# Kernel tuning notes

Measured on AMD Instinct MI355X. Metric: run time of the kernel, lower is better.

Reference implementation:

```python
import jax, jax.numpy as jnp
import numpy as np

N_NODES = 100000
N_EDGES = 1600000
IN_CH, HID_CH, OUT_CH = 128, 128, 64


def _sage_conv(x, src, dst, Wl, bl, Wr, num_nodes):
    # PyG SAGEConv (aggr='mean', root_weight=True):
    #   out_i = W_l @ mean_{j in N(i)} x_j + b_l + W_r @ x_i
    msgs = x[src]                                            # [E, d] gather
    agg = jax.ops.segment_sum(msgs, dst, num_segments=num_nodes)   # [N, d]
    cnt = jax.ops.segment_sum(jnp.ones((src.shape[0],), x.dtype), dst,
                              num_segments=num_nodes)              # [N]
    mean = agg / jnp.maximum(cnt, 1.0)[:, None]
    return mean @ Wl.T + bl + x @ Wr.T


def setup_inputs() -> dict:
    key = jax.random.key(0)
    ks = jax.random.split(key, 8)
    x = jax.random.normal(ks[0], (N_NODES, IN_CH), dtype=jnp.float32)
    edge_index = jax.random.randint(ks[1], (2, N_EDGES), 0, N_NODES, dtype=jnp.int32)
    s1 = 1.0 / np.sqrt(IN_CH)
    s2 = 1.0 / np.sqrt(HID_CH)
    Wl1 = jax.random.uniform(ks[2], (HID_CH, IN_CH), jnp.float32, -s1, s1)
    bl1 = jax.random.uniform(ks[3], (HID_CH,), jnp.float32, -s1, s1)
    Wr1 = jax.random.uniform(ks[4], (HID_CH, IN_CH), jnp.float32, -s1, s1)
    Wl2 = jax.random.uniform(ks[5], (OUT_CH, HID_CH), jnp.float32, -s2, s2)
    bl2 = jax.random.uniform(ks[6], (OUT_CH,), jnp.float32, -s2, s2)
    Wr2 = jax.random.uniform(ks[7], (OUT_CH, HID_CH), jnp.float32, -s2, s2)
    return {"x": x, "edge_index": edge_index, "Wl1": Wl1, "bl1": bl1,
            "Wr1": Wr1, "Wl2": Wl2, "bl2": bl2, "Wr2": Wr2}


def reference(x, edge_index, Wl1, bl1, Wr1, Wl2, bl2, Wr2):
    src, dst = edge_index[0], edge_index[1]
    n = x.shape[0]
    h = _sage_conv(x, src, dst, Wl1, bl1, Wr1, n)
    h = jax.nn.relu(h)  # dropout is identity in eval mode
    out = _sage_conv(h, src, dst, Wl2, bl2, Wr2, n)
    return out
```

## Files before the change

### kernel.cpp

```cpp
#include <hip/hip_runtime.h>
#include <hip/hip_bf16.h>
#include <stdint.h>

#define IN_CH 128
#define NPB   448
#define NBUCK 224
#define CAP   8192
#define PART_EPB 2048
#define SRC_BITS 17
#define SRC_MASK ((1 << SRC_BITS) - 1)

typedef short v8s __attribute__((ext_vector_type(8)));
typedef float v4f __attribute__((ext_vector_type(4)));

__device__ __forceinline__ ushort f2b(float f) {
    return ((__hip_bfloat16_raw)__float2bfloat16(f)).x;
}
__device__ __forceinline__ float b2f(ushort u) {
    __hip_bfloat16_raw r; r.x = u;
    return __bfloat162float((__hip_bfloat16)r);
}

__global__ __launch_bounds__(256) void k_part(
    const int* __restrict__ src, const int* __restrict__ dst,
    int* __restrict__ cursor, int* __restrict__ ebuf, int E) {
    __shared__ int sedge[PART_EPB];
    __shared__ int h[NBUCK], lofs[NBUCK], gbase[NBUCK], lcur[NBUCK];
    __shared__ int ssc[256];

    int tid = threadIdx.x;
    int eb0 = blockIdx.x * PART_EPB;
    int cnt = min(PART_EPB, E - eb0);

    if (tid < NBUCK) { h[tid] = 0; lcur[tid] = 0; }
    __syncthreads();
    for (int i = tid; i < cnt; i += 256)
        atomicAdd(&h[dst[eb0 + i] / NPB], 1);
    __syncthreads();
    int v = (tid < NBUCK) ? h[tid] : 0;
    ssc[tid] = v;
    __syncthreads();
    for (int off = 1; off < 256; off <<= 1) {
        int val = (tid >= off) ? ssc[tid - off] : 0;
        __syncthreads();
        ssc[tid] += val;
        __syncthreads();
    }
    int excl = ssc[tid] - v;
    if (tid < NBUCK) {
        lofs[tid] = excl;
        gbase[tid] = tid * CAP + atomicAdd(&cursor[tid], v);
    }
    __syncthreads();
    for (int i = tid; i < cnt; i += 256) {
        int s0 = src[eb0 + i];
        int d0 = dst[eb0 + i];
        int b = d0 / NPB;
        int dl = d0 - b * NPB;
        int p = atomicAdd(&lcur[b], 1);
        sedge[lofs[b] + p] = (dl << SRC_BITS) | s0;
    }
    __syncthreads();
    for (int i = tid; i < cnt; i += 256) {
        int lo = 0, hi = NBUCK - 1;
        while (lo < hi) {
            int mid = (lo + hi + 1) >> 1;
            if (lofs[mid] <= i) lo = mid; else hi = mid - 1;
        }
        int pos = gbase[lo] + (i - lofs[lo]);
        if (pos < (lo + 1) * CAP) ebuf[pos] = sedge[i];
    }
}

__global__ __launch_bounds__(256) void k_bbuild(
    const int* __restrict__ ebuf, const int* __restrict__ cursor,
    int* __restrict__ row_ptr, int* __restrict__ deg,
    int* __restrict__ col, int N) {
    __shared__ int sdeg[NPB];
    __shared__ int scur[NPB];
    __shared__ int ssum[256];
    int b = blockIdx.x, tid = threadIdx.x;
    int base = b * NPB;
    int nodes = min(NPB, N - base);
    int e0 = b * CAP;
    int e1 = e0 + min(cursor[b], CAP);

    for (int i = tid; i < NPB; i += 256) sdeg[i] = 0;
    __syncthreads();
    for (int e = e0 + tid; e < e1; e += 256)
        atomicAdd(&sdeg[((unsigned)ebuf[e]) >> SRC_BITS], 1);
    __syncthreads();
    int d0 = 0, d1 = 0;
    if (tid < 224) { d0 = sdeg[2 * tid]; d1 = sdeg[2 * tid + 1]; }
    int ts = d0 + d1;
    ssum[tid] = ts;
    __syncthreads();
    for (int off = 1; off < 256; off <<= 1) {
        int val = (tid >= off) ? ssum[tid - off] : 0;
        __syncthreads();
        ssum[tid] += val;
        __syncthreads();
    }
    int excl = ssum[tid] - ts;
    if (tid < 224) {
        scur[2 * tid] = excl;
        scur[2 * tid + 1] = excl + d0;
        if (2 * tid < nodes) {
            row_ptr[base + 2 * tid] = e0 + excl;
            deg[base + 2 * tid] = d0;
        }
        if (2 * tid + 1 < nodes) {
            row_ptr[base + 2 * tid + 1] = e0 + excl + d0;
            deg[base + 2 * tid + 1] = d1;
        }
    }
    __syncthreads();
    for (int e = e0 + tid; e < e1; e += 256) {
        int w = ebuf[e];
        int dl = ((unsigned)w) >> SRC_BITS;
        int p = atomicAdd(&scur[dl], 1);
        col[e0 + p] = w & SRC_MASK;
    }
}

template <int OC, int MODE>
__global__ __launch_bounds__(256) void k_wgemm(
    const float* __restrict__ Af, const ushort* __restrict__ Ab,
    const float* __restrict__ WlF, const float* __restrict__ WrF,
    ushort* __restrict__ qb, ushort* __restrict__ pbb, float* __restrict__ pbf,
    int N) {
    const int NT = OC / 16;
    const int LDW = 128 + 8;
    __shared__ ushort Wlds[OC * LDW];

    int tid = threadIdx.x;
    for (int it = 0; it < OC / 16; it++) {
        int idx = it * 256 + tid;
        int r = idx >> 4, kc = (idx & 15) * 8;
        const float* Wrow = (r < OC / 2) ? (WlF + (size_t)r * 128)
                                         : (WrF + (size_t)(r - OC / 2) * 128);
        float4 w0 = *(const float4*)(Wrow + kc);
        float4 w1 = *(const float4*)(Wrow + kc + 4);
        v8s wv;
        wv[0] = (short)f2b(w0.x); wv[1] = (short)f2b(w0.y);
        wv[2] = (short)f2b(w0.z); wv[3] = (short)f2b(w0.w);
        wv[4] = (short)f2b(w1.x); wv[5] = (short)f2b(w1.y);
        wv[6] = (short)f2b(w1.z); wv[7] = (short)f2b(w1.w);
        *(v8s*)((short*)Wlds + r * LDW + kc) = wv;
    }
    __syncthreads();

    int wave = tid >> 6;
    int lane = tid & 63;
    int m16 = lane & 15;
    int quad = lane >> 4;
    int rowbase = blockIdx.x * 128 + wave * 32;

    v4f acc[2][NT];
#pragma unroll
    for (int mt = 0; mt < 2; mt++)
#pragma unroll
        for (int t = 0; t < NT; t++) acc[mt][t] = {0.f, 0.f, 0.f, 0.f};

    int ar0 = min(rowbase + m16, N - 1);
    int ar1 = min(rowbase + 16 + m16, N - 1);

#pragma unroll
    for (int ks = 0; ks < 4; ks++) {
        int k0 = ks * 32 + quad * 8;
        v8s a0, a1;
        if (MODE == 0) {
            float4 f00 = *(const float4*)(Af + (size_t)ar0 * 128 + k0);
            float4 f01 = *(const float4*)(Af + (size_t)ar0 * 128 + k0 + 4);
            float4 f10 = *(const float4*)(Af + (size_t)ar1 * 128 + k0);
            float4 f11 = *(const float4*)(Af + (size_t)ar1 * 128 + k0 + 4);
            a0[0] = (short)f2b(f00.x); a0[1] = (short)f2b(f00.y);
            a0[2] = (short)f2b(f00.z); a0[3] = (short)f2b(f00.w);
            a0[4] = (short)f2b(f01.x); a0[5] = (short)f2b(f01.y);
            a0[6] = (short)f2b(f01.z); a0[7] = (short)f2b(f01.w);
            a1[0] = (short)f2b(f10.x); a1[1] = (short)f2b(f10.y);
            a1[2] = (short)f2b(f10.z); a1[3] = (short)f2b(f10.w);
            a1[4] = (short)f2b(f11.x); a1[5] = (short)f2b(f11.y);
            a1[6] = (short)f2b(f11.z); a1[7] = (short)f2b(f11.w);
        } else {
            a0 = *(const v8s*)((const short*)Ab + (size_t)ar0 * 128 + k0);
            a1 = *(const v8s*)((const short*)Ab + (size_t)ar1 * 128 + k0);
        }
#pragma unroll
        for (int t = 0; t < NT; t++) {
            v8s b = *(const v8s*)((const short*)Wlds + (t * 16 + m16) * LDW + k0);
            acc[0][t] = __builtin_amdgcn_mfma_f32_16x16x32_bf16(a0, b, acc[0][t], 0, 0, 0);
            acc[1][t] = __builtin_amdgcn_mfma_f32_16x16x32_bf16(a1, b, acc[1][t], 0, 0, 0);
        }
    }

#pragma unroll
    for (int mt = 0; mt < 2; mt++) {
        int orow0 = rowbase + mt * 16 + quad * 4;
#pragma unroll
        for (int r = 0; r < 4; r++) {
            int orow = orow0 + r;
            if (orow < N) {
#pragma unroll
                for (int t = 0; t < NT; t++) {
                    int c = t * 16 + m16;
                    float v = acc[mt][t][r];
                    if (MODE == 0) {
                        if (c < 128) qb[(size_t)orow * 128 + c] = f2b(v);
                        else pbb[(size_t)orow * 128 + (c - 128)] = f2b(v);
                    } else {
                        if (c < 64) qb[(size_t)orow * 64 + c] = f2b(v);
                        else pbf[(size_t)orow * 64 + (c - 64)] = v;
                    }
                }
            }
        }
    }
}

__global__ void k_agg1(const int* __restrict__ row_ptr, const int* __restrict__ deg,
                       const int* __restrict__ col, const ushort* __restrict__ q1b,
                       const ushort* __restrict__ p1b, const float* __restrict__ bias,
                       ushort* __restrict__ hb, int N) {
    int node = blockIdx.x * (blockDim.x >> 6) + (threadIdx.x >> 6);
    int lane = threadIdx.x & 63;
    if (node >= N) return;
    int s0 = row_ptr[node];
    int dn = deg[node];
    int s1 = s0 + dn;
    int ch = 2 * lane;
    float ax = 0.f, ay = 0.f;
    int j = s0;
    for (; j + 8 <= s1; j += 8) {
        int c0 = col[j],     c1 = col[j + 1], c2 = col[j + 2], c3 = col[j + 3];
        int c4 = col[j + 4], c5 = col[j + 5], c6 = col[j + 6], c7 = col[j + 7];
        ushort2 v0 = *(const ushort2*)(q1b + (size_t)c0 * 128 + ch);
        ushort2 v1 = *(const ushort2*)(q1b + (size_t)c1 * 128 + ch);
        ushort2 v2 = *(const ushort2*)(q1b + (size_t)c2 * 128 + ch);
        ushort2 v3 = *(const ushort2*)(q1b + (size_t)c3 * 128 + ch);
        ushort2 v4 = *(const ushort2*)(q1b + (size_t)c4 * 128 + ch);
        ushort2 v5 = *(const ushort2*)(q1b + (size_t)c5 * 128 + ch);
        ushort2 v6 = *(const ushort2*)(q1b + (size_t)c6 * 128 + ch);
        ushort2 v7 = *(const ushort2*)(q1b + (size_t)c7 * 128 + ch);
        ax += b2f(v0.x) + b2f(v1.x) + b2f(v2.x) + b2f(v3.x)
            + b2f(v4.x) + b2f(v5.x) + b2f(v6.x) + b2f(v7.x);
        ay += b2f(v0.y) + b2f(v1.y) + b2f(v2.y) + b2f(v3.y)
            + b2f(v4.y) + b2f(v5.y) + b2f(v6.y) + b2f(v7.y);
    }
    for (; j < s1; j++) {
        ushort2 v = *(const ushort2*)(q1b + (size_t)col[j] * 128 + ch);
        ax += b2f(v.x); ay += b2f(v.y);
    }
    float inv = (dn > 0) ? 1.0f / (float)dn : 0.0f;
    ushort2 pb = *(const ushort2*)(p1b + (size_t)node * 128 + ch);
    float2 bi = *(const float2*)(bias + ch);
    ushort2 o;
    o.x = f2b(fmaxf(ax * inv + b2f(pb.x) + bi.x, 0.f));
    o.y = f2b(fmaxf(ay * inv + b2f(pb.y) + bi.y, 0.f));
    *(ushort2*)(hb + (size_t)node * 128 + ch) = o;
}

__global__ void k_agg2(const int* __restrict__ row_ptr, const int* __restrict__ deg,
                       const int* __restrict__ col, const ushort* __restrict__ q2,
                       const float* __restrict__ p2, const float* __restrict__ bias,
                       float* __restrict__ out, int N) {
    int node = blockIdx.x * (blockDim.x >> 6) + (threadIdx.x >> 6);
    int lane = threadIdx.x & 63;
    if (node >= N) return;
    int s0 = row_ptr[node];
    int dn = deg[node];
    int s1 = s0 + dn;
    int half = lane >> 5, cl = lane & 31;
    int ch = 2 * cl;
    float ax = 0.f, ay = 0.f;
    int j = s0;
    for (; j + 16 <= s1; j += 16) {
        int c0 = col[j + half],      c1 = col[j + 2 + half];
        int c2 = col[j + 4 + half],  c3 = col[j + 6 + half];
        int c4 = col[j + 8 + half],  c5 = col[j + 10 + half];
        int c6 = col[j + 12 + half], c7 = col[j + 14 + half];
        ushort2 v0 = *(const ushort2*)(q2 + (size_t)c0 * 64 + ch);
        ushort2 v1 = *(const ushort2*)(q2 + (size_t)c1 * 64 + ch);
        ushort2 v2 = *(const ushort2*)(q2 + (size_t)c2 * 64 + ch);
        ushort2 v3 = *(const ushort2*)(q2 + (size_t)c3 * 64 + ch);
        ushort2 v4 = *(const ushort2*)(q2 + (size_t)c4 * 64 + ch);
        ushort2 v5 = *(const ushort2*)(q2 + (size_t)c5 * 64 + ch);
        ushort2 v6 = *(const ushort2*)(q2 + (size_t)c6 * 64 + ch);
        ushort2 v7 = *(const ushort2*)(q2 + (size_t)c7 * 64 + ch);
        ax += b2f(v0.x) + b2f(v1.x) + b2f(v2.x) + b2f(v3.x)
            + b2f(v4.x) + b2f(v5.x) + b2f(v6.x) + b2f(v7.x);
        ay += b2f(v0.y) + b2f(v1.y) + b2f(v2.y) + b2f(v3.y)
            + b2f(v4.y) + b2f(v5.y) + b2f(v6.y) + b2f(v7.y);
    }
    for (; j + half < s1; j += 2) {
        ushort2 v = *(const ushort2*)(q2 + (size_t)col[j + half] * 64 + ch);
        ax += b2f(v.x); ay += b2f(v.y);
    }
    ax += __shfl_xor(ax, 32);
    ay += __shfl_xor(ay, 32);
    if (half == 0) {
        float inv = (dn > 0) ? 1.0f / (float)dn : 0.0f;
        float2 pv = *(const float2*)(p2 + (size_t)node * 64 + ch);
        float2 bi = *(const float2*)(bias + ch);
        float2 o;
        o.x = ax * inv + pv.x + bi.x;
        o.y = ay * inv + pv.y + bi.y;
        *(float2*)(out + (size_t)node * 64 + ch) = o;
    }
}

extern "C" void kernel_launch(void* const* d_in, const int* in_sizes, int n_in,
                              void* d_out, int out_size, void* d_ws, size_t ws_size,
                              hipStream_t stream) {
    const float* x   = (const float*)d_in[0];
    const int* ei    = (const int*)d_in[1];
    const float* Wl1 = (const float*)d_in[2];
    const float* bl1 = (const float*)d_in[3];
    const float* Wr1 = (const float*)d_in[4];
    const float* Wl2 = (const float*)d_in[5];
    const float* bl2 = (const float*)d_in[6];
    const float* Wr2 = (const float*)d_in[7];

    const int N = in_sizes[0] / IN_CH;
    const int E = in_sizes[1] / 2;
    const int* src = ei;
    const int* dst = ei + E;

    char* p = (char*)d_ws;
    auto carve = [&](size_t bytes) -> void* {
        void* q = (void*)p;
        p += (bytes + 255) & ~(size_t)255;
        return q;
    };
    int* cursor   = (int*)carve(NBUCK * 4);
    int* ebuf     = (int*)carve((size_t)NBUCK * CAP * 4);
    int* col      = (int*)carve((size_t)NBUCK * CAP * 4);
    int* row_ptr  = (int*)carve((size_t)N * 4);
    int* deg      = (int*)carve((size_t)N * 4);
    ushort* q1b   = (ushort*)carve((size_t)N * 128 * 2);
    ushort* p1b   = (ushort*)carve((size_t)N * 128 * 2);
    ushort* hb    = (ushort*)carve((size_t)N * 128 * 2);
    ushort* q2    = (ushort*)carve((size_t)N * 64 * 2);
    float* p2     = (float*)carve((size_t)N * 64 * 4);
    (void)ws_size; (void)n_in;

    float* out = (float*)d_out;
    (void)out_size;

    (void)hipMemsetAsync(cursor, 0, NBUCK * 4, stream);
    k_part<<<(E + PART_EPB - 1) / PART_EPB, 256, 0, stream>>>(src, dst, cursor, ebuf, E);
    k_bbuild<<<NBUCK, 256, 0, stream>>>(ebuf, cursor, row_ptr, deg, col, N);

    k_wgemm<256, 0><<<(N + 127) / 128, 256, 0, stream>>>(
        x, nullptr, Wl1, Wr1, q1b, p1b, nullptr, N);
    k_agg1<<<(N + 3) / 4, 256, 0, stream>>>(row_ptr, deg, col, q1b, p1b, bl1, hb, N);

    k_wgemm<128, 1><<<(N + 127) / 128, 256, 0, stream>>>(
        nullptr, hb, Wl2, Wr2, q2, nullptr, p2, N);
    k_agg2<<<(N + 3) / 4, 256, 0, stream>>>(row_ptr, deg, col, q2, p2, bl2, out, N);
}
```

Measured before the change: 335.9 us.

## Split layer-1 gather table into 64-channel planes and vectorize GEMM epilogue stores

```diff
diff --git a/kernel.cpp b/kernel.cpp
--- a/kernel.cpp
+++ b/kernel.cpp
@@ -72,50 +72,43 @@
     }
 }
 
-__global__ __launch_bounds__(256) void k_bbuild(
+__global__ __launch_bounds__(512) void k_bbuild(
     const int* __restrict__ ebuf, const int* __restrict__ cursor,
     int* __restrict__ row_ptr, int* __restrict__ deg,
     int* __restrict__ col, int N) {
     __shared__ int sdeg[NPB];
     __shared__ int scur[NPB];
-    __shared__ int ssum[256];
+    __shared__ int ssum[512];
     int b = blockIdx.x, tid = threadIdx.x;
     int base = b * NPB;
     int nodes = min(NPB, N - base);
     int e0 = b * CAP;
     int e1 = e0 + min(cursor[b], CAP);
 
-    for (int i = tid; i < NPB; i += 256) sdeg[i] = 0;
-    __syncthreads();
-    for (int e = e0 + tid; e < e1; e += 256)
+    if (tid < NPB) sdeg[tid] = 0;
+    __syncthreads();
+    for (int e = e0 + tid; e < e1; e += 512)
         atomicAdd(&sdeg[((unsigned)ebuf[e]) >> SRC_BITS], 1);
     __syncthreads();
-    int d0 = 0, d1 = 0;
-    if (tid < 224) { d0 = sdeg[2 * tid]; d1 = sdeg[2 * tid + 1]; }
-    int ts = d0 + d1;
-    ssum[tid] = ts;
-    __syncthreads();
-    for (int off = 1; off < 256; off <<= 1) {
+    int v = (tid < NPB) ? sdeg[tid] : 0;
+    ssum[tid] = v;
+    __syncthreads();
+    for (int off = 1; off < 512; off <<= 1) {
         int val = (tid >= off) ? ssum[tid - off] : 0;
         __syncthreads();
         ssum[tid] += val;
         __syncthreads();
     }
-    int excl = ssum[tid] - ts;
-    if (tid < 224) {
-        scur[2 * tid] = excl;
-        scur[2 * tid + 1] = excl + d0;
-        if (2 * tid < nodes) {
-            row_ptr[base + 2 * tid] = e0 + excl;
-            deg[base + 2 * tid] = d0;
-        }
-        if (2 * tid + 1 < nodes) {
-            row_ptr[base + 2 * tid + 1] = e0 + excl + d0;
-            deg[base + 2 * tid + 1] = d1;
-        }
-    }
-    __syncthreads();
-    for (int e = e0 + tid; e < e1; e += 256) {
+    int excl = ssum[tid] - v;
+    if (tid < NPB) {
+        scur[tid] = excl;
+        if (tid < nodes) {
+            row_ptr[base + tid] = e0 + excl;
+            deg[base + tid] = v;
+        }
+    }
+    __syncthreads();
+    for (int e = e0 + tid; e < e1; e += 512) {
         int w = ebuf[e];
         int dl = ((unsigned)w) >> SRC_BITS;
         int p = atomicAdd(&scur[dl], 1);
@@ -127,8 +120,8 @@
 __global__ __launch_bounds__(256) void k_wgemm(
     const float* __restrict__ Af, const ushort* __restrict__ Ab,
     const float* __restrict__ WlF, const float* __restrict__ WrF,
-    ushort* __restrict__ qb, ushort* __restrict__ pbb, float* __restrict__ pbf,
-    int N) {
+    ushort* __restrict__ q1, ushort* __restrict__ p1,
+    ushort* __restrict__ q2, float* __restrict__ p2, int N) {
     const int NT = OC / 16;
     const int LDW = 128 + 8;
     __shared__ ushort Wlds[OC * LDW];
@@ -168,49 +161,61 @@
 #pragma unroll
     for (int ks = 0; ks < 4; ks++) {
         int k0 = ks * 32 + quad * 8;
-        v8s a0, a1;
+        v8s b0, b1;
         if (MODE == 0) {
             float4 f00 = *(const float4*)(Af + (size_t)ar0 * 128 + k0);
             float4 f01 = *(const float4*)(Af + (size_t)ar0 * 128 + k0 + 4);
             float4 f10 = *(const float4*)(Af + (size_t)ar1 * 128 + k0);
             float4 f11 = *(const float4*)(Af + (size_t)ar1 * 128 + k0 + 4);
-            a0[0] = (short)f2b(f00.x); a0[1] = (short)f2b(f00.y);
-            a0[2] = (short)f2b(f00.z); a0[3] = (short)f2b(f00.w);
-            a0[4] = (short)f2b(f01.x); a0[5] = (short)f2b(f01.y);
-            a0[6] = (short)f2b(f01.z); a0[7] = (short)f2b(f01.w);
-            a1[0] = (short)f2b(f10.x); a1[1] = (short)f2b(f10.y);
-            a1[2] = (short)f2b(f10.z); a1[3] = (short)f2b(f10.w);
-            a1[4] = (short)f2b(f11.x); a1[5] = (short)f2b(f11.y);
-            a1[6] = (short)f2b(f11.z); a1[7] = (short)f2b(f11.w);
+            b0[0] = (short)f2b(f00.x); b0[1] = (short)f2b(f00.y);
+            b0[2] = (short)f2b(f00.z); b0[3] = (short)f2b(f00.w);
+            b0[4] = (short)f2b(f01.x); b0[5] = (short)f2b(f01.y);
+            b0[6] = (short)f2b(f01.z); b0[7] = (short)f2b(f01.w);
+            b1[0] = (short)f2b(f10.x); b1[1] = (short)f2b(f10.y);
+            b1[2] = (short)f2b(f10.z); b1[3] = (short)f2b(f10.w);
+            b1[4] = (short)f2b(f11.x); b1[5] = (short)f2b(f11.y);
+            b1[6] = (short)f2b(f11.z); b1[7] = (short)f2b(f11.w);
         } else {
-            a0 = *(const v8s*)((const short*)Ab + (size_t)ar0 * 128 + k0);
-            a1 = *(const v8s*)((const short*)Ab + (size_t)ar1 * 128 + k0);
+            b0 = *(const v8s*)((const short*)Ab + (size_t)ar0 * 128 + k0);
+            b1 = *(const v8s*)((const short*)Ab + (size_t)ar1 * 128 + k0);
         }
 #pragma unroll
         for (int t = 0; t < NT; t++) {
-            v8s b = *(const v8s*)((const short*)Wlds + (t * 16 + m16) * LDW + k0);
-            acc[0][t] = __builtin_amdgcn_mfma_f32_16x16x32_bf16(a0, b, acc[0][t], 0, 0, 0);
-            acc[1][t] = __builtin_amdgcn_mfma_f32_16x16x32_bf16(a1, b, acc[1][t], 0, 0, 0);
+            v8s aW = *(const v8s*)((const short*)Wlds + (t * 16 + m16) * LDW + k0);
+            acc[0][t] = __builtin_amdgcn_mfma_f32_16x16x32_bf16(aW, b0, acc[0][t], 0, 0, 0);
+            acc[1][t] = __builtin_amdgcn_mfma_f32_16x16x32_bf16(aW, b1, acc[1][t], 0, 0, 0);
         }
     }
 
 #pragma unroll
     for (int mt = 0; mt < 2; mt++) {
-        int orow0 = rowbase + mt * 16 + quad * 4;
-#pragma unroll
-        for (int r = 0; r < 4; r++) {
-            int orow = orow0 + r;
-            if (orow < N) {
-#pragma unroll
-                for (int t = 0; t < NT; t++) {
-                    int c = t * 16 + m16;
-                    float v = acc[mt][t][r];
-                    if (MODE == 0) {
-                        if (c < 128) qb[(size_t)orow * 128 + c] = f2b(v);
-                        else pbb[(size_t)orow * 128 + (c - 128)] = f2b(v);
+        int node = rowbase + mt * 16 + m16;
+        if (node < N) {
+#pragma unroll
+            for (int t = 0; t < NT; t++) {
+                int c0 = t * 16 + quad * 4;
+                float v0 = acc[mt][t][0], v1 = acc[mt][t][1];
+                float v2 = acc[mt][t][2], v3 = acc[mt][t][3];
+                if (MODE == 0) {
+                    if (c0 < 128) {
+                        ushort4 o;
+                        o.x = f2b(v0); o.y = f2b(v1); o.z = f2b(v2); o.w = f2b(v3);
+                        int plane = c0 >> 6;
+                        *(ushort4*)(q1 + (size_t)plane * N * 64 +
+                                    (size_t)node * 64 + (c0 & 63)) = o;
                     } else {
-                        if (c < 64) qb[(size_t)orow * 64 + c] = f2b(v);
-                        else pbf[(size_t)orow * 64 + (c - 64)] = v;
+                        ushort4 o;
+                        o.x = f2b(v0); o.y = f2b(v1); o.z = f2b(v2); o.w = f2b(v3);
+                        *(ushort4*)(p1 + (size_t)node * 128 + (c0 - 128)) = o;
+                    }
+                } else {
+                    if (c0 < 64) {
+                        ushort4 o;
+                        o.x = f2b(v0); o.y = f2b(v1); o.z = f2b(v2); o.w = f2b(v3);
+                        *(ushort4*)(q2 + (size_t)node * 64 + c0) = o;
+                    } else {
+                        float4 o = {v0, v1, v2, v3};
+                        *(float4*)(p2 + (size_t)node * 64 + (c0 - 64)) = o;
                     }
                 }
             }
@@ -219,45 +224,52 @@
 }
 
 __global__ void k_agg1(const int* __restrict__ row_ptr, const int* __restrict__ deg,
-                       const int* __restrict__ col, const ushort* __restrict__ q1b,
-                       const ushort* __restrict__ p1b, const float* __restrict__ bias,
-                       ushort* __restrict__ hb, int N) {
+                       const int* __restrict__ col, const ushort* __restrict__ qpl,
+                       const ushort* __restrict__ p1, const float* __restrict__ bias,
+                       ushort* __restrict__ hb, int N, int chbase) {
     int node = blockIdx.x * (blockDim.x >> 6) + (threadIdx.x >> 6);
     int lane = threadIdx.x & 63;
     if (node >= N) return;
     int s0 = row_ptr[node];
     int dn = deg[node];
     int s1 = s0 + dn;
-    int ch = 2 * lane;
+    int half = lane >> 5, cl = lane & 31;
+    int ch = 2 * cl;
     float ax = 0.f, ay = 0.f;
     int j = s0;
-    for (; j + 8 <= s1; j += 8) {
-        int c0 = col[j],     c1 = col[j + 1], c2 = col[j + 2], c3 = col[j + 3];
-        int c4 = col[j + 4], c5 = col[j + 5], c6 = col[j + 6], c7 = col[j + 7];
-        ushort2 v0 = *(const ushort2*)(q1b + (size_t)c0 * 128 + ch);
-        ushort2 v1 = *(const ushort2*)(q1b + (size_t)c1 * 128 + ch);
-        ushort2 v2 = *(const ushort2*)(q1b + (size_t)c2 * 128 + ch);
-        ushort2 v3 = *(const ushort2*)(q1b + (size_t)c3 * 128 + ch);
-        ushort2 v4 = *(const ushort2*)(q1b + (size_t)c4 * 128 + ch);
-        ushort2 v5 = *(const ushort2*)(q1b + (size_t)c5 * 128 + ch);
-        ushort2 v6 = *(const ushort2*)(q1b + (size_t)c6 * 128 + ch);
-        ushort2 v7 = *(const ushort2*)(q1b + (size_t)c7 * 128 + ch);
+    for (; j + 16 <= s1; j += 16) {
+        int c0 = col[j + half],      c1 = col[j + 2 + half];
+        int c2 = col[j + 4 + half],  c3 = col[j + 6 + half];
+        int c4 = col[j + 8 + half],  c5 = col[j + 10 + half];
+        int c6 = col[j + 12 + half], c7 = col[j + 14 + half];
+        ushort2 v0 = *(const ushort2*)(qpl + (size_t)c0 * 64 + ch);
+        ushort2 v1 = *(const ushort2*)(qpl + (size_t)c1 * 64 + ch);
+        ushort2 v2 = *(const ushort2*)(qpl + (size_t)c2 * 64 + ch);
+        ushort2 v3 = *(const ushort2*)(qpl + (size_t)c3 * 64 + ch);
+        ushort2 v4 = *(const ushort2*)(qpl + (size_t)c4 * 64 + ch);
+        ushort2 v5 = *(const ushort2*)(qpl + (size_t)c5 * 64 + ch);
+        ushort2 v6 = *(const ushort2*)(qpl + (size_t)c6 * 64 + ch);
+        ushort2 v7 = *(const ushort2*)(qpl + (size_t)c7 * 64 + ch);
         ax += b2f(v0.x) + b2f(v1.x) + b2f(v2.x) + b2f(v3.x)
             + b2f(v4.x) + b2f(v5.x) + b2f(v6.x) + b2f(v7.x);
         ay += b2f(v0.y) + b2f(v1.y) + b2f(v2.y) + b2f(v3.y)
             + b2f(v4.y) + b2f(v5.y) + b2f(v6.y) + b2f(v7.y);
     }
-    for (; j < s1; j++) {
-        ushort2 v = *(const ushort2*)(q1b + (size_t)col[j] * 128 + ch);
+    for (; j + half < s1; j += 2) {
+        ushort2 v = *(const ushort2*)(qpl + (size_t)col[j + half] * 64 + ch);
         ax += b2f(v.x); ay += b2f(v.y);
     }
-    float inv = (dn > 0) ? 1.0f / (float)dn : 0.0f;
-    ushort2 pb = *(const ushort2*)(p1b + (size_t)node * 128 + ch);
-    float2 bi = *(const float2*)(bias + ch);
-    ushort2 o;
-    o.x = f2b(fmaxf(ax * inv + b2f(pb.x) + bi.x, 0.f));
-    o.y = f2b(fmaxf(ay * inv + b2f(pb.y) + bi.y, 0.f));
-    *(ushort2*)(hb + (size_t)node * 128 + ch) = o;
+    ax += __shfl_xor(ax, 32);
+    ay += __shfl_xor(ay, 32);
+    if (half == 0) {
+        float inv = (dn > 0) ? 1.0f / (float)dn : 0.0f;
+        ushort2 pb = *(const ushort2*)(p1 + (size_t)node * 128 + chbase + ch);
+        float2 bi = *(const float2*)(bias + chbase + ch);
+        ushort2 o;
+        o.x = f2b(fmaxf(ax * inv + b2f(pb.x) + bi.x, 0.f));
+        o.y = f2b(fmaxf(ay * inv + b2f(pb.y) + bi.y, 0.f));
+        *(ushort2*)(hb + (size_t)node * 128 + chbase + ch) = o;
+    }
 }
 
 __global__ void k_agg2(const int* __restrict__ row_ptr, const int* __restrict__ deg,
@@ -337,8 +349,8 @@
     int* col      = (int*)carve((size_t)NBUCK * CAP * 4);
     int* row_ptr  = (int*)carve((size_t)N * 4);
     int* deg      = (int*)carve((size_t)N * 4);
-    ushort* q1b   = (ushort*)carve((size_t)N * 128 * 2);
-    ushort* p1b   = (ushort*)carve((size_t)N * 128 * 2);
+    ushort* q1    = (ushort*)carve((size_t)2 * N * 64 * 2);
+    ushort* p1    = (ushort*)carve((size_t)N * 128 * 2);
     ushort* hb    = (ushort*)carve((size_t)N * 128 * 2);
     ushort* q2    = (ushort*)carve((size_t)N * 64 * 2);
     float* p2     = (float*)carve((size_t)N * 64 * 4);
@@ -349,13 +361,16 @@
 
     (void)hipMemsetAsync(cursor, 0, NBUCK * 4, stream);
     k_part<<<(E + PART_EPB - 1) / PART_EPB, 256, 0, stream>>>(src, dst, cursor, ebuf, E);
-    k_bbuild<<<NBUCK, 256, 0, stream>>>(ebuf, cursor, row_ptr, deg, col, N);
+    k_bbuild<<<NBUCK, 512, 0, stream>>>(ebuf, cursor, row_ptr, deg, col, N);
 
     k_wgemm<256, 0><<<(N + 127) / 128, 256, 0, stream>>>(
-        x, nullptr, Wl1, Wr1, q1b, p1b, nullptr, N);
-    k_agg1<<<(N + 3) / 4, 256, 0, stream>>>(row_ptr, deg, col, q1b, p1b, bl1, hb, N);
+        x, nullptr, Wl1, Wr1, q1, p1, nullptr, nullptr, N);
+    k_agg1<<<(N + 3) / 4, 256, 0, stream>>>(
+        row_ptr, deg, col, q1, p1, bl1, hb, N, 0);
+    k_agg1<<<(N + 3) / 4, 256, 0, stream>>>(
+        row_ptr, deg, col, q1 + (size_t)N * 64, p1, bl1, hb, N, 64);
 
     k_wgemm<128, 1><<<(N + 127) / 128, 256, 0, stream>>>(
-        nullptr, hb, Wl2, Wr2, q2, nullptr, p2, N);
+        nullptr, hb, Wl2, Wr2, nullptr, nullptr, q2, p2, N);
     k_agg2<<<(N + 3) / 4, 256, 0, stream>>>(row_ptr, deg, col, q2, p2, bl2, out, N);
 }
```

Result: slower. 400.9 us (+19.4%).
